# Kernel tuning notes

Hardware: AMD Instinct MI355X
Metric: run time of the kernel (lower is better)

## Reference

```python
import jax, jax.numpy as jnp
import numpy as np

EPS = 1e-5
NEG_SLOPE = 0.01  # torch leaky_relu default


def _layer_norm(x, g, b):
    m = jnp.mean(x, axis=-1, keepdims=True)
    v = jnp.var(x, axis=-1, keepdims=True)
    return (x - m) * jax.lax.rsqrt(v + EPS) * g + b


def setup_inputs() -> dict:
    key = jax.random.key(0)
    ks = jax.random.split(key, 8)
    bs, n, c, out_c, enc_dim = 8, 2048, 128, 128, 64
    s = 1.0 / np.sqrt(c)
    return {
        "x": jax.random.normal(ks[0], (bs, n, c), jnp.float32),
        "enc": jax.random.normal(ks[1], (bs, n, enc_dim), jnp.float32),
        "W_enc": jax.random.uniform(ks[2], (c, enc_dim), jnp.float32, -1, 1) / np.sqrt(enc_dim),
        "b_enc": jnp.zeros((c,), jnp.float32),
        "g1": jnp.ones((c,), jnp.float32),
        "b1": jnp.zeros((c,), jnp.float32),
        "g2": jnp.ones((c,), jnp.float32),
        "b2": jnp.zeros((c,), jnp.float32),
        "W0": jax.random.uniform(ks[3], (c, c), jnp.float32, -1, 1) * s,
        "Wa": jax.random.uniform(ks[4], (2 * c,), jnp.float32, -1, 1) / np.sqrt(2 * c),
        "W1": jax.random.uniform(ks[5], (out_c, c), jnp.float32, -1, 1) * s,
    }


def reference(x, enc, W_enc, b_enc, g1, b1, g2, b2, W0, Wa, W1):
    c = x.shape[-1]
    k = 1
    # positional encoding projection
    x = x + enc @ W_enc.T + b_enc
    x_norm = _layer_norm(x, g1, b1)
    # head i=0 (k=1)
    h = x_norm @ W0.T  # [bs, n, c]
    # GAT attention: e[b,i,j] = leaky_relu(a . cat(h_i, h_j)) computed via split weights
    a1, a2 = Wa[:c], Wa[c:]
    s1 = h @ a1  # [bs, n] contribution of node i
    s2 = h @ a2  # [bs, n] contribution of node j
    e = jax.nn.leaky_relu(s1[:, :, None] + s2[:, None, :], NEG_SLOPE)  # [bs, n, n]
    atten = jax.nn.softmax(e, axis=2)
    attentioned = jnp.einsum("bij,bjc->bic", atten, h)
    attentioned = attentioned + x  # residual
    attentioned = _layer_norm(attentioned, g2, b2)
    h_next = jax.nn.elu(attentioned @ W1.T) / k
    atten_agg = jax.lax.stop_gradient(atten) / k
    return h_next, atten_agg
```

## Files before the change

### kernel.cpp

```cpp
#include <hip/hip_runtime.h>
#include <hip/hip_bf16.h>
#include <cstddef>

#define EPS 1e-5f
#define NSLOPE 0.01f

typedef __attribute__((ext_vector_type(8))) short s16x8;
typedef __attribute__((ext_vector_type(4))) float f32x4;

union BF8 { unsigned short u[8]; s16x8 v; };

static __device__ inline unsigned short f2bf(float f) {
    unsigned int u = __float_as_uint(f);
    u += 0x7fffu + ((u >> 16) & 1u);
    return (unsigned short)(u >> 16);
}

__global__ __launch_bounds__(256) void kW(
    const float* __restrict__ W_enc, const float* __restrict__ W0,
    const float* __restrict__ W1,
    unsigned short* __restrict__ Web, unsigned short* __restrict__ W0b,
    unsigned short* __restrict__ W1b)
{
    int idx = blockIdx.x * 256 + threadIdx.x;
    if (idx < 128 * 64) Web[idx] = f2bf(W_enc[idx]);
    if (idx < 128 * 128) { W0b[idx] = f2bf(W0[idx]); W1b[idx] = f2bf(W1[idx]); }
}

__global__ __launch_bounds__(256, 4) void kA(
    const float* __restrict__ x, const float* __restrict__ enc,
    const unsigned short* __restrict__ Web, const float* __restrict__ b_enc,
    const float* __restrict__ g1, const float* __restrict__ b1,
    const unsigned short* __restrict__ W0b, const float* __restrict__ Wa,
    float* __restrict__ xnew, unsigned short* __restrict__ hP,
    float* __restrict__ s1, float* __restrict__ s2)
{
    __shared__ float ys[32][132];
    __shared__ unsigned short xnb[32][136];
    __shared__ unsigned short hts[128][40];
    __shared__ float ps1[2][32], ps2[2][32];

    int t = threadIdx.x;
    int w = t >> 6, lane = t & 63;
    int ml = lane & 15, quad = lane >> 4;
    int mrow = (w & 1) * 16;
    int chalf = (w >> 1) * 64;
    long long R0 = (long long)blockIdx.x * 32;
    int b = (int)(R0 >> 11);
    int jt = (int)((R0 & 2047) >> 5);

    f32x4 acc1[4] = {};
    const float* encrow = enc + (R0 + mrow + ml) * 64 + quad * 8;
#pragma unroll
    for (int kb = 0; kb < 2; ++kb) {
        float4 e0 = *(const float4*)(encrow + kb * 32);
        float4 e1 = *(const float4*)(encrow + kb * 32 + 4);
        BF8 af;
        af.u[0] = f2bf(e0.x); af.u[1] = f2bf(e0.y);
        af.u[2] = f2bf(e0.z); af.u[3] = f2bf(e0.w);
        af.u[4] = f2bf(e1.x); af.u[5] = f2bf(e1.y);
        af.u[6] = f2bf(e1.z); af.u[7] = f2bf(e1.w);
#pragma unroll
        for (int ct = 0; ct < 4; ++ct) {
            int n = chalf + ct * 16 + ml;
            s16x8 bf = *(const s16x8*)(Web + n * 64 + kb * 32 + quad * 8);
            acc1[ct] = __builtin_amdgcn_mfma_f32_16x16x32_bf16(af.v, bf, acc1[ct], 0, 0, 0);
        }
    }
#pragma unroll
    for (int ct = 0; ct < 4; ++ct) {
        int col = chalf + ct * 16 + ml;
        float be = b_enc[col];
#pragma unroll
        for (int rg = 0; rg < 4; ++rg) {
            int rl = mrow + quad * 4 + rg;
            long long row = R0 + rl;
            float y = acc1[ct][rg] + x[row * 128 + col] + be;
            xnew[row * 128 + col] = y;
            ys[rl][col] = y;
        }
    }
    __syncthreads();

    {
        int rl = t >> 3, sub = t & 7;
        float v[16];
        float s = 0.f, q = 0.f;
#pragma unroll
        for (int i = 0; i < 16; ++i) {
            v[i] = ys[rl][sub * 16 + i];
            s += v[i]; q += v[i] * v[i];
        }
#pragma unroll
        for (int m = 1; m < 8; m <<= 1) { s += __shfl_xor(s, m); q += __shfl_xor(q, m); }
        float mean = s * (1.f / 128.f);
        float var = q * (1.f / 128.f) - mean * mean;
        float rstd = rsqrtf(var + EPS);
#pragma unroll
        for (int i = 0; i < 16; ++i) {
            int col = sub * 16 + i;
            float xn = (v[i] - mean) * rstd * g1[col] + b1[col];
            xnb[rl][col] = f2bf(xn);
        }
    }
    __syncthreads();

    f32x4 acc2[4] = {};
#pragma unroll
    for (int kb = 0; kb < 4; ++kb) {
        s16x8 af = *(const s16x8*)(&xnb[mrow + ml][kb * 32 + quad * 8]);
#pragma unroll
        for (int ct = 0; ct < 4; ++ct) {
            int n = chalf + ct * 16 + ml;
            s16x8 bf = *(const s16x8*)(W0b + n * 128 + kb * 32 + quad * 8);
            acc2[ct] = __builtin_amdgcn_mfma_f32_16x16x32_bf16(af, bf, acc2[ct], 0, 0, 0);
        }
    }

#pragma unroll
    for (int ct = 0; ct < 4; ++ct) {
        int col = chalf + ct * 16 + ml;
#pragma unroll
        for (int rg = 0; rg < 4; ++rg)
            hts[col][mrow + quad * 4 + rg] = f2bf(acc2[ct][rg]);
    }
#pragma unroll
    for (int rg = 0; rg < 4; ++rg) {
        float p1 = 0.f, p2 = 0.f;
#pragma unroll
        for (int ct = 0; ct < 4; ++ct) {
            int col = chalf + ct * 16 + ml;
            p1 += acc2[ct][rg] * Wa[col];
            p2 += acc2[ct][rg] * Wa[128 + col];
        }
#pragma unroll
        for (int m = 1; m < 16; m <<= 1) { p1 += __shfl_xor(p1, m); p2 += __shfl_xor(p2, m); }
        if (ml == 0) {
            int rl = mrow + quad * 4 + rg;
            ps1[w >> 1][rl] = p1;
            ps2[w >> 1][rl] = p2;
        }
    }
    __syncthreads();
    if (t < 32) {
        s1[R0 + t] = ps1[0][t] + ps1[1][t];
        s2[R0 + t] = ps2[0][t] + ps2[1][t];
    }
    {
        int c = t >> 1, half = t & 1;
        unsigned short* dst = hP + (((long long)b * 64 + jt) * 128 + c) * 32 + half * 16;
        const unsigned short* srcp = &hts[c][half * 16];
        *(s16x8*)(dst) = *(const s16x8*)(srcp);
        *(s16x8*)(dst + 8) = *(const s16x8*)(srcp + 8);
    }
}

__global__ __launch_bounds__(256) void kC(const float* __restrict__ s1,
                                          const float* __restrict__ s2,
                                          float* __restrict__ Cc)
{
    int t = threadIdx.x;
    int w = t >> 6, lane = t & 63;
    long long row = (long long)blockIdx.x * 4 + w;
    int b = (int)(row >> 11);
    const float* s2b = s2 + (long long)b * 2048;
    float s1i = s1[row];

    float mx = -1e30f;
    for (int j = lane; j < 2048; j += 64) mx = fmaxf(mx, s2b[j]);
    for (int m = 32; m; m >>= 1) mx = fmaxf(mx, __shfl_xor(mx, m));
    float z0 = s1i + mx;
    float mi = fmaxf(z0, NSLOPE * z0);

    float l = 0.f;
    for (int j = lane; j < 2048; j += 64) {
        float z = s1i + s2b[j];
        float zl = fmaxf(z, NSLOPE * z);
        l += __expf(zl - mi);
    }
    for (int m = 32; m; m >>= 1) l += __shfl_xor(l, m);
    if (lane == 0) Cc[row] = mi + __logf(l);
}

__global__ __launch_bounds__(256, 4) void kD(
    const float* __restrict__ s1, const float* __restrict__ s2,
    const float* __restrict__ Cc, const unsigned short* __restrict__ hP,
    float* __restrict__ atten, float* __restrict__ attn)
{
    __shared__ float Pt[2][16][36];
    __shared__ float R[2][16][68];

    int t = threadIdx.x;
    int w = t >> 6, lane = t & 63;
    int jh = w & 1, ch = w >> 1;
    int chalf = ch * 64;
    int b = blockIdx.x >> 7;
    int it = blockIdx.x & 127;
    int i0 = it * 16;
    int ml = lane & 15, quad = lane >> 4;

    long long gi = (long long)b * 2048 + i0 + ml;
    float s1i = s1[gi];
    float Ci = Cc[gi];
    const float* s2b = s2 + (long long)b * 2048;
    const unsigned short* hPb = hP + (long long)b * 64 * 128 * 32;

    int sr = lane >> 3, sc = lane & 7;
    float* abase = atten + ((long long)b * 2048 + i0) * 2048;

    f32x4 acc[4] = {};
    for (int jj = 0; jj < 1024; jj += 32) {
        int j0 = jh * 1024 + jj;
        int jb = j0 + quad * 8;
        float4 sa = *(const float4*)(s2b + jb);
        float4 sb = *(const float4*)(s2b + jb + 4);
        float zs[8] = {sa.x, sa.y, sa.z, sa.w, sb.x, sb.y, sb.z, sb.w};
        float p[8];
        BF8 af;
#pragma unroll
        for (int k = 0; k < 8; ++k) {
            float z = s1i + zs[k];
            float zl = fmaxf(z, NSLOPE * z);
            p[k] = __expf(zl - Ci);
            af.u[k] = f2bf(p[k]);
        }
        if (ch == 0) {
            *(f32x4*)&Pt[jh][ml][quad * 8]     = *(const f32x4*)&p[0];
            *(f32x4*)&Pt[jh][ml][quad * 8 + 4] = *(const f32x4*)&p[4];
            f32x4 r0 = *(const f32x4*)&Pt[jh][sr][sc * 4];
            f32x4 r1 = *(const f32x4*)&Pt[jh][8 + sr][sc * 4];
            *(f32x4*)(abase + (long long)sr * 2048 + j0 + sc * 4) = r0;
            *(f32x4*)(abase + (long long)(8 + sr) * 2048 + j0 + sc * 4) = r1;
        }
        const unsigned short* tb = hPb + (long long)(j0 >> 5) * 128 * 32;
#pragma unroll
        for (int ct = 0; ct < 4; ++ct) {
            s16x8 bfrag = *(const s16x8*)(tb + (chalf + ct * 16 + ml) * 32 + quad * 8);
            acc[ct] = __builtin_amdgcn_mfma_f32_16x16x32_bf16(af.v, bfrag, acc[ct], 0, 0, 0);
        }
    }

    if (jh == 1) {
#pragma unroll
        for (int ct = 0; ct < 4; ++ct)
#pragma unroll
            for (int rg = 0; rg < 4; ++rg)
                R[ch][quad * 4 + rg][ct * 16 + ml] = acc[ct][rg];
    }
    __syncthreads();
    if (jh == 0) {
#pragma unroll
        for (int ct = 0; ct < 4; ++ct) {
#pragma unroll
            for (int rg = 0; rg < 4; ++rg) {
                int ii = quad * 4 + rg;
                float v = acc[ct][rg] + R[ch][ii][ct * 16 + ml];
                attn[((long long)b * 2048 + i0 + ii) * 128 + chalf + ct * 16 + ml] = v;
            }
        }
    }
}

__global__ __launch_bounds__(256, 4) void kE(
    const float* __restrict__ xnew, const float* __restrict__ g2,
    const float* __restrict__ b2, const unsigned short* __restrict__ W1b,
    float* __restrict__ io)
{
    __shared__ unsigned short xnb[32][136];
    int t = threadIdx.x;
    long long R0 = (long long)blockIdx.x * 32;

    {
        int rl = t >> 3, sub = t & 7;
        long long row = R0 + rl;
        const float* pio = io + row * 128 + sub * 16;
        const float* pxn = xnew + row * 128 + sub * 16;
        float v[16];
        float s = 0.f, q = 0.f;
#pragma unroll
        for (int i = 0; i < 16; i += 4) {
            float4 a = *(const float4*)(pio + i);
            float4 c = *(const float4*)(pxn + i);
            v[i]     = a.x + c.x; v[i + 1] = a.y + c.y;
            v[i + 2] = a.z + c.z; v[i + 3] = a.w + c.w;
        }
#pragma unroll
        for (int i = 0; i < 16; ++i) { s += v[i]; q += v[i] * v[i]; }
#pragma unroll
        for (int m = 1; m < 8; m <<= 1) { s += __shfl_xor(s, m); q += __shfl_xor(q, m); }
        float mean = s * (1.f / 128.f);
        float var = q * (1.f / 128.f) - mean * mean;
        float rstd = rsqrtf(var + EPS);
#pragma unroll
        for (int i = 0; i < 16; ++i) {
            int col = sub * 16 + i;
            float xn = (v[i] - mean) * rstd * g2[col] + b2[col];
            xnb[rl][col] = f2bf(xn);
        }
    }
    __syncthreads();

    int w = t >> 6, lane = t & 63;
    int ml = lane & 15, quad = lane >> 4;
    int mrow = (w & 1) * 16;
    int chalf = (w >> 1) * 64;

    f32x4 acc[4] = {};
#pragma unroll
    for (int kb = 0; kb < 4; ++kb) {
        s16x8 af = *(const s16x8*)(&xnb[mrow + ml][kb * 32 + quad * 8]);
#pragma unroll
        for (int ct = 0; ct < 4; ++ct) {
            int n = chalf + ct * 16 + ml;
            s16x8 bf = *(const s16x8*)(W1b + n * 128 + kb * 32 + quad * 8);
            acc[ct] = __builtin_amdgcn_mfma_f32_16x16x32_bf16(af, bf, acc[ct], 0, 0, 0);
        }
    }
#pragma unroll
    for (int ct = 0; ct < 4; ++ct) {
        int col = chalf + ct * 16 + ml;
#pragma unroll
        for (int rg = 0; rg < 4; ++rg) {
            int rl = mrow + quad * 4 + rg;
            float h = acc[ct][rg];
            float o = h > 0.f ? h : (__expf(h) - 1.f);
            io[(R0 + rl) * 128 + col] = o;
        }
    }
}

extern "C" void kernel_launch(void* const* d_in, const int* in_sizes, int n_in,
                              void* d_out, int out_size, void* d_ws, size_t ws_size,
                              hipStream_t stream)
{
    const float* x     = (const float*)d_in[0];
    const float* enc   = (const float*)d_in[1];
    const float* W_enc = (const float*)d_in[2];
    const float* b_enc = (const float*)d_in[3];
    const float* g1    = (const float*)d_in[4];
    const float* b1    = (const float*)d_in[5];
    const float* g2    = (const float*)d_in[6];
    const float* b2    = (const float*)d_in[7];
    const float* W0    = (const float*)d_in[8];
    const float* Wa    = (const float*)d_in[9];
    const float* W1    = (const float*)d_in[10];

    float* out = (float*)d_out;
    const long long ROWS = 8LL * 2048;
    const long long HN   = ROWS * 128;

    float* xnew = (float*)d_ws;
    float* s1   = xnew + HN;
    float* s2   = s1 + ROWS;
    float* Cc   = s2 + ROWS;
    unsigned short* hP  = (unsigned short*)(Cc + ROWS);
    unsigned short* Web = hP + HN;
    unsigned short* W0b = Web + 128 * 64;
    unsigned short* W1b = W0b + 128 * 128;

    float* atten = out + HN;
    float* attn  = out;

    kW<<<64, 256, 0, stream>>>(W_enc, W0, W1, Web, W0b, W1b);
    kA<<<512, 256, 0, stream>>>(x, enc, Web, b_enc, g1, b1, W0b, Wa,
                                xnew, hP, s1, s2);
    kC<<<4096, 256, 0, stream>>>(s1, s2, Cc);
    kD<<<1024, 256, 0, stream>>>(s1, s2, Cc, hP, atten, attn);
    kE<<<512, 256, 0, stream>>>(xnew, g2, b2, W1b, out);
}
```

Baseline: 238.3 us.

## Fuse softmax normalizer into attention kernel, split j across four waves, nontemporal stores

Removes the separate kC launch by computing the per-row log-sum-exp normalizer at the start of kD, with each wave handling four of the block's 16 rows. The j-range is now split across all four waves, each covering all 128 channels, and partial results are reduced through a larger shared buffer. All waves now write attention probabilities using nontemporal stores, so the large atten output bypasses cache retention. The cost is extra per-block work (each block rereads s2 for the max and exp sums), more accumulator registers, and more shared memory.

```diff
diff --git a/kernel.cpp b/kernel.cpp
--- a/kernel.cpp
+++ b/kernel.cpp
@@ -14,6 +14,10 @@
     unsigned int u = __float_as_uint(f);
     u += 0x7fffu + ((u >> 16) & 1u);
     return (unsigned short)(u >> 16);
+}
+
+static __device__ inline void nt_store4(float* p, f32x4 v) {
+    __builtin_nontemporal_store(v, (f32x4*)p);
 }
 
 __global__ __launch_bounds__(256) void kW(
@@ -155,62 +159,55 @@
     }
 }
 
-__global__ __launch_bounds__(256) void kC(const float* __restrict__ s1,
-                                          const float* __restrict__ s2,
-                                          float* __restrict__ Cc)
-{
+__global__ __launch_bounds__(256, 4) void kD(
+    const float* __restrict__ s1, const float* __restrict__ s2,
+    const unsigned short* __restrict__ hP,
+    float* __restrict__ atten, float* __restrict__ attn)
+{
+    __shared__ float Pt[4][16][36];
+    __shared__ float Rbuf[3][16][132];
+    __shared__ float s1sh[16], Csh[16];
+
     int t = threadIdx.x;
     int w = t >> 6, lane = t & 63;
-    long long row = (long long)blockIdx.x * 4 + w;
-    int b = (int)(row >> 11);
-    const float* s2b = s2 + (long long)b * 2048;
-    float s1i = s1[row];
-
-    float mx = -1e30f;
-    for (int j = lane; j < 2048; j += 64) mx = fmaxf(mx, s2b[j]);
-    for (int m = 32; m; m >>= 1) mx = fmaxf(mx, __shfl_xor(mx, m));
-    float z0 = s1i + mx;
-    float mi = fmaxf(z0, NSLOPE * z0);
-
-    float l = 0.f;
-    for (int j = lane; j < 2048; j += 64) {
-        float z = s1i + s2b[j];
-        float zl = fmaxf(z, NSLOPE * z);
-        l += __expf(zl - mi);
-    }
-    for (int m = 32; m; m >>= 1) l += __shfl_xor(l, m);
-    if (lane == 0) Cc[row] = mi + __logf(l);
-}
-
-__global__ __launch_bounds__(256, 4) void kD(
-    const float* __restrict__ s1, const float* __restrict__ s2,
-    const float* __restrict__ Cc, const unsigned short* __restrict__ hP,
-    float* __restrict__ atten, float* __restrict__ attn)
-{
-    __shared__ float Pt[2][16][36];
-    __shared__ float R[2][16][68];
-
-    int t = threadIdx.x;
-    int w = t >> 6, lane = t & 63;
-    int jh = w & 1, ch = w >> 1;
-    int chalf = ch * 64;
     int b = blockIdx.x >> 7;
     int it = blockIdx.x & 127;
     int i0 = it * 16;
     int ml = lane & 15, quad = lane >> 4;
 
-    long long gi = (long long)b * 2048 + i0 + ml;
-    float s1i = s1[gi];
-    float Ci = Cc[gi];
     const float* s2b = s2 + (long long)b * 2048;
+
+    float mxs = -1e30f;
+    for (int j = lane; j < 2048; j += 64) mxs = fmaxf(mxs, s2b[j]);
+#pragma unroll
+    for (int m = 32; m; m >>= 1) mxs = fmaxf(mxs, __shfl_xor(mxs, m));
+#pragma unroll
+    for (int r = 0; r < 4; ++r) {
+        int rl = w * 4 + r;
+        float s1i = s1[(long long)b * 2048 + i0 + rl];
+        float z0 = s1i + mxs;
+        float mi = fmaxf(z0, NSLOPE * z0);
+        float l = 0.f;
+        for (int j = lane; j < 2048; j += 64) {
+            float z = s1i + s2b[j];
+            float zl = fmaxf(z, NSLOPE * z);
+            l += __expf(zl - mi);
+        }
+#pragma unroll
+        for (int m = 32; m; m >>= 1) l += __shfl_xor(l, m);
+        if (lane == 0) { s1sh[rl] = s1i; Csh[rl] = mi + __logf(l); }
+    }
+    __syncthreads();
+
+    float s1i = s1sh[ml];
+    float Ci  = Csh[ml];
     const unsigned short* hPb = hP + (long long)b * 64 * 128 * 32;
-
     int sr = lane >> 3, sc = lane & 7;
     float* abase = atten + ((long long)b * 2048 + i0) * 2048;
 
-    f32x4 acc[4] = {};
-    for (int jj = 0; jj < 1024; jj += 32) {
-        int j0 = jh * 1024 + jj;
+    f32x4 acc[8] = {};
+    for (int jj = 0; jj < 512; jj += 32) {
+        int j0 = w * 512 + jj;
         int jb = j0 + quad * 8;
         float4 sa = *(const float4*)(s2b + jb);
         float4 sb = *(const float4*)(s2b + jb + 4);
@@ -224,38 +221,39 @@
             p[k] = __expf(zl - Ci);
             af.u[k] = f2bf(p[k]);
         }
-        if (ch == 0) {
-            *(f32x4*)&Pt[jh][ml][quad * 8]     = *(const f32x4*)&p[0];
-            *(f32x4*)&Pt[jh][ml][quad * 8 + 4] = *(const f32x4*)&p[4];
-            f32x4 r0 = *(const f32x4*)&Pt[jh][sr][sc * 4];
-            f32x4 r1 = *(const f32x4*)&Pt[jh][8 + sr][sc * 4];
-            *(f32x4*)(abase + (long long)sr * 2048 + j0 + sc * 4) = r0;
-            *(f32x4*)(abase + (long long)(8 + sr) * 2048 + j0 + sc * 4) = r1;
-        }
+        *(f32x4*)&Pt[w][ml][quad * 8]     = *(const f32x4*)&p[0];
+        *(f32x4*)&Pt[w][ml][quad * 8 + 4] = *(const f32x4*)&p[4];
+        f32x4 r0 = *(const f32x4*)&Pt[w][sr][sc * 4];
+        f32x4 r1 = *(const f32x4*)&Pt[w][8 + sr][sc * 4];
+        nt_store4(abase + (long long)sr * 2048 + j0 + sc * 4, r0);
+        nt_store4(abase + (long long)(8 + sr) * 2048 + j0 + sc * 4, r1);
+
         const unsigned short* tb = hPb + (long long)(j0 >> 5) * 128 * 32;
 #pragma unroll
-        for (int ct = 0; ct < 4; ++ct) {
-            s16x8 bfrag = *(const s16x8*)(tb + (chalf + ct * 16 + ml) * 32 + quad * 8);
+        for (int ct = 0; ct < 8; ++ct) {
+            s16x8 bfrag = *(const s16x8*)(tb + (ct * 16 + ml) * 32 + quad * 8);
             acc[ct] = __builtin_amdgcn_mfma_f32_16x16x32_bf16(af.v, bfrag, acc[ct], 0, 0, 0);
         }
     }
 
-    if (jh == 1) {
-#pragma unroll
-        for (int ct = 0; ct < 4; ++ct)
+    if (w > 0) {
+#pragma unroll
+        for (int ct = 0; ct < 8; ++ct)
 #pragma unroll
             for (int rg = 0; rg < 4; ++rg)
-                R[ch][quad * 4 + rg][ct * 16 + ml] = acc[ct][rg];
-    }
-    __syncthreads();
-    if (jh == 0) {
-#pragma unroll
-        for (int ct = 0; ct < 4; ++ct) {
+                Rbuf[w - 1][quad * 4 + rg][ct * 16 + ml] = acc[ct][rg];
+    }
+    __syncthreads();
+    if (w == 0) {
+#pragma unroll
+        for (int ct = 0; ct < 8; ++ct) {
 #pragma unroll
             for (int rg = 0; rg < 4; ++rg) {
                 int ii = quad * 4 + rg;
-                float v = acc[ct][rg] + R[ch][ii][ct * 16 + ml];
-                attn[((long long)b * 2048 + i0 + ii) * 128 + chalf + ct * 16 + ml] = v;
+                int cc = ct * 16 + ml;
+                float v = acc[ct][rg] + Rbuf[0][ii][cc] + Rbuf[1][ii][cc]
+                        + Rbuf[2][ii][cc];
+                attn[((long long)b * 2048 + i0 + ii) * 128 + cc] = v;
             }
         }
     }
@@ -352,8 +350,7 @@
     float* xnew = (float*)d_ws;
     float* s1   = xnew + HN;
     float* s2   = s1 + ROWS;
-    float* Cc   = s2 + ROWS;
-    unsigned short* hP  = (unsigned short*)(Cc + ROWS);
+    unsigned short* hP  = (unsigned short*)(s2 + ROWS);
     unsigned short* Web = hP + HN;
     unsigned short* W0b = Web + 128 * 64;
     unsigned short* W1b = W0b + 128 * 128;
@@ -364,7 +361,6 @@
     kW<<<64, 256, 0, stream>>>(W_enc, W0, W1, Web, W0b, W1b);
     kA<<<512, 256, 0, stream>>>(x, enc, Web, b_enc, g1, b1, W0b, Wa,
                                 xnew, hP, s1, s2);
-    kC<<<4096, 256, 0, stream>>>(s1, s2, Cc);
-    kD<<<1024, 256, 0, stream>>>(s1, s2, Cc, hP, atten, attn);
+    kD<<<1024, 256, 0, stream>>>(s1, s2, hP, atten, attn);
     kE<<<512, 256, 0, stream>>>(xnew, g2, b2, W1b, out);
 }
```

Result: faster. 233.4 us (-2.1%).
